# Kernel tuning notes

Measured on AMD Instinct MI355X. Metric: run time of the kernel, lower is better.

Reference implementation:

```python
import jax, jax.numpy as jnp
import numpy as np

B, N, K = 2, 2048, 30          # batch, residues, neighbors
DN, DE, L = 256, 128, 3        # dim_nodes, dim_edges, num_layers
NF, EF = 12, 28                # raw node / edge feature dims
EPS = 1e-6


def _gather(h, idx):
    # h: [B,N,D], idx: [B,N,K] -> [B,N,K,D]
    b, n, k = idx.shape
    d = h.shape[-1]
    return jnp.take_along_axis(h, idx.reshape(b, n * k, 1), axis=1).reshape(b, n, k, d)


def _nrm(v):
    return v / (jnp.linalg.norm(v, axis=-1, keepdims=True) + EPS)


def _forward(X, C, Wn, bn, We, be, Wm1, bm1, Wm2, bm2, Wue1, bue1, Wue2, bue2):
    mask_i = (C > 0).astype(X.dtype)                      # [B,N]
    Nat, CA, Cat, Oat = X[..., 0, :], X[..., 1, :], X[..., 2, :], X[..., 3, :]

    # local residue frames via Gram-Schmidt on (N, CA, C)
    u = _nrm(Cat - CA)
    v0 = Nat - CA
    v = _nrm(v0 - jnp.sum(v0 * u, -1, keepdims=True) * u)
    w = jnp.cross(u, v)
    R = jnp.stack([u, v, w], axis=-1)                     # [B,N,3,3]

    # node features: internal coords (unit bond vectors + log lengths)
    def bond_feat(bv):
        return jnp.concatenate([_nrm(bv), jnp.log(jnp.linalg.norm(bv, axis=-1, keepdims=True) + EPS)], -1)
    node_feat = jnp.concatenate([bond_feat(CA - Nat), bond_feat(Cat - CA), bond_feat(Oat - Cat)], -1)  # [B,N,12]
    node_h = (node_feat @ Wn + bn) * mask_i[..., None]

    # kNN graph on centroid distances (graph_distance_atom_type=-1)
    Xc = X.mean(axis=2)                                   # [B,N,3]
    D2 = jnp.sum((Xc[:, :, None] - Xc[:, None, :]) ** 2, -1)  # [B,N,N]
    BIG = 1e9
    D2 = D2 + BIG * (1.0 - mask_i)[:, None, :] + BIG * jnp.eye(N, dtype=X.dtype)[None]
    _, edge_idx = jax.lax.top_k(-D2, K)                   # [B,N,K]

    mask_j = _gather(mask_i[..., None], edge_idx)[..., 0]
    mask_ij = mask_i[..., None] * mask_j                  # [B,N,K]

    # edge features: RBF distances + local-frame direction + relative rotation
    xj = _gather(Xc, edge_idx)
    d = xj - Xc[:, :, None]                               # [B,N,K,3]
    dist = jnp.linalg.norm(d, axis=-1)
    local = jnp.einsum('bndc,bnkd->bnkc', R, d)           # R_i^T d
    dirv = local / (dist[..., None] + EPS)
    Rj = _gather(R.reshape(B, N, 9), edge_idx).reshape(B, N, K, 3, 3)
    Rrel = jnp.einsum('bnde,bnkdf->bnkef', R, Rj).reshape(B, N, K, 9)  # R_i^T R_j
    centers = jnp.linspace(0.0, 20.0, 16)
    sigma = 20.0 / 16.0
    rbf = jnp.exp(-(((dist[..., None] - centers) / sigma) ** 2))       # [B,N,K,16]
    edge_h = (jnp.concatenate([rbf, dirv, Rrel], -1) @ We + be) * mask_ij[..., None]

    # GNN message passing: gather -> MLP -> masked mean scatter, + edge update
    denom = jnp.sum(mask_ij, -1, keepdims=True) + EPS     # [B,N,1]
    for l in range(L):
        hj = _gather(node_h, edge_idx)                    # [B,N,K,DN]
        hi = jnp.broadcast_to(node_h[:, :, None], hj.shape)
        mi = jnp.concatenate([hi, hj, edge_h], -1)        # [B,N,K,2*DN+DE]
        m = jax.nn.softplus(mi @ Wm1[l] + bm1[l]) @ Wm2[l] + bm2[l]
        m = m * mask_ij[..., None]
        node_h = (node_h + m.sum(axis=2) / denom) * mask_i[..., None]
        e = jax.nn.softplus(mi @ Wue1[l] + bue1[l]) @ Wue2[l] + bue2[l]
        edge_h = (edge_h + e) * mask_ij[..., None]

    return node_h, edge_h, edge_idx, mask_i, mask_ij


def setup_inputs() -> dict:
    key = jax.random.key(0)
    ks = jax.random.split(key, 10)
    s = lambda i, shp: jax.random.normal(ks[i], shp, jnp.float32) * 0.05
    M = 2 * DN + DE
    inp = {
        'X': jax.random.normal(ks[0], (B, N, 4, 3), jnp.float32),
        'C': jax.random.randint(ks[1], (B, N), 0, 4),
        'Wn': s(2, (NF, DN)), 'bn': jnp.zeros((DN,), jnp.float32),
        'We': s(3, (EF, DE)), 'be': jnp.zeros((DE,), jnp.float32),
        'Wm1': s(4, (L, M, DN)), 'bm1': jnp.zeros((L, DN), jnp.float32),
        'Wm2': s(5, (L, DN, DN)), 'bm2': jnp.zeros((L, DN), jnp.float32),
        'Wue1': s(6, (L, M, DE)), 'bue1': jnp.zeros((L, DE), jnp.float32),
        'Wue2': s(7, (L, DE, DE)), 'bue2': jnp.zeros((L, DE), jnp.float32),
    }
    return inp


def reference(X, C, Wn, bn, We, be, Wm1, bm1, Wm2, bm2, Wue1, bue1, Wue2, bue2):
    return _forward(X, C, Wn, bn, We, be, Wm1, bm1, Wm2, bm2, Wue1, bue1, Wue2, bue2)
```

## Files before the change

kernel.cpp:

```cpp
#include <hip/hip_runtime.h>
#include <math.h>

#define Bdim 2
#define Nn   2048
#define Kn   30
#define KP   32
#define DNc  256
#define DEc  128
#define NODES (Bdim*Nn)
#define EDGES (Bdim*Nn*Kn)
#define RPAD  (NODES*KP)
#define EPSF 1e-6f

#define BK 64
#define LDA (BK+8)
#define LDP 136

typedef __attribute__((ext_vector_type(8))) short short8;
typedef __attribute__((ext_vector_type(4))) short sh4;
typedef __attribute__((ext_vector_type(4))) float floatx4;

__device__ __forceinline__ float softplusf(float x){
    float e = __expf(-fabsf(x));
    return fmaxf(x, 0.f) + __logf(1.f + e);
}

__device__ __forceinline__ unsigned short f2bf(float x){
    union { float f; unsigned u; } v; v.f = x;
    unsigned r = v.u + 0x7fff + ((v.u >> 16) & 1);
    return (unsigned short)(r >> 16);
}
__device__ __forceinline__ float bf2f(unsigned short h){
    union { unsigned u; float f; } v; v.u = ((unsigned)h) << 16;
    return v.f;
}

__global__ __launch_bounds__(256) void k_geom(
    const float* __restrict__ X, const int* __restrict__ C,
    float* __restrict__ Xc, float* __restrict__ Rm,
    float* __restrict__ feat, float* __restrict__ mask_out)
{
    int id = blockIdx.x*256 + threadIdx.x;
    if (id >= NODES) return;
    float a[4][3];
    #pragma unroll
    for (int t=0;t<4;++t)
        #pragma unroll
        for (int d=0;d<3;++d) a[t][d] = X[id*12 + t*3 + d];
    #pragma unroll
    for (int d=0; d<3; ++d){
        float s = __fadd_rn(__fadd_rn(__fadd_rn(a[0][d],a[1][d]),a[2][d]),a[3][d]);
        Xc[id*3+d] = __fmul_rn(s, 0.25f);
    }
    mask_out[id] = (C[id] > 0) ? 1.f : 0.f;

    float u[3], v[3], w[3], b2[3], v0[3], vv[3];
    #pragma unroll
    for (int d=0;d<3;++d) b2[d] = a[2][d]-a[1][d];
    float n2 = sqrtf(b2[0]*b2[0]+b2[1]*b2[1]+b2[2]*b2[2]);
    #pragma unroll
    for (int d=0;d<3;++d) u[d] = b2[d]/(n2+EPSF);
    #pragma unroll
    for (int d=0;d<3;++d) v0[d] = a[0][d]-a[1][d];
    float dt = v0[0]*u[0]+v0[1]*u[1]+v0[2]*u[2];
    #pragma unroll
    for (int d=0;d<3;++d) vv[d] = v0[d] - dt*u[d];
    float nv = sqrtf(vv[0]*vv[0]+vv[1]*vv[1]+vv[2]*vv[2]);
    #pragma unroll
    for (int d=0;d<3;++d) v[d] = vv[d]/(nv+EPSF);
    w[0] = u[1]*v[2]-u[2]*v[1];
    w[1] = u[2]*v[0]-u[0]*v[2];
    w[2] = u[0]*v[1]-u[1]*v[0];
    #pragma unroll
    for (int d=0;d<3;++d){
        Rm[id*9 + d*3 + 0] = u[d];
        Rm[id*9 + d*3 + 1] = v[d];
        Rm[id*9 + d*3 + 2] = w[d];
    }
    float bonds[3][3];
    #pragma unroll
    for (int d=0;d<3;++d){
        bonds[0][d] = a[1][d]-a[0][d];
        bonds[1][d] = b2[d];
        bonds[2][d] = a[3][d]-a[2][d];
    }
    #pragma unroll
    for (int bi=0;bi<3;++bi){
        float nb = sqrtf(bonds[bi][0]*bonds[bi][0]+bonds[bi][1]*bonds[bi][1]+bonds[bi][2]*bonds[bi][2]);
        #pragma unroll
        for (int d=0;d<3;++d) feat[id*12 + bi*4 + d] = bonds[bi][d]/(nb+EPSF);
        feat[id*12 + bi*4 + 3] = logf(nb+EPSF);
    }
}

__global__ __launch_bounds__(256) void k_nodeh(
    const float* __restrict__ feat, const float* __restrict__ Wn,
    const float* __restrict__ bn, const int* __restrict__ C,
    float* __restrict__ node_h, unsigned short* __restrict__ node_bf)
{
    int nid = blockIdx.x;
    int c   = threadIdx.x;
    __shared__ float f[12];
    if (c < 12) f[c] = feat[nid*12 + c];
    __syncthreads();
    float acc = bn[c];
    #pragma unroll
    for (int k=0;k<12;++k) acc += f[k]*Wn[k*DNc + c];
    float mask = (C[nid] > 0) ? 1.f : 0.f;
    float r = acc*mask;
    node_h[nid*DNc + c] = r;
    node_bf[nid*DNc + c] = f2bf(r);
}

__global__ __launch_bounds__(256) void k_knn(
    const float* __restrict__ Xc, const int* __restrict__ C,
    int* __restrict__ eidx, float* __restrict__ eidx_f)
{
    __shared__ float sx[Nn], sy[Nn], sz[Nn], sadd[Nn];
    int tid  = threadIdx.x;
    int lane = tid & 63, wave = tid >> 6;
    int node0 = blockIdx.x*4;
    int base  = (node0 >> 11) << 11;
    for (int j=tid; j<Nn; j+=256){
        int gj = base + j;
        sx[j] = Xc[gj*3+0]; sy[j] = Xc[gj*3+1]; sz[j] = Xc[gj*3+2];
        sadd[j] = (C[gj] > 0) ? 0.f : 1e9f;
    }
    __syncthreads();

    int node = node0 + wave;
    int iloc = node & (Nn-1);
    float xi = sx[iloc], yi = sy[iloc], zi = sz[iloc];

    unsigned long long kreg[32];
    unsigned long long gm[8];
    #pragma unroll
    for (int t=0; t<32; ++t){
        int j = lane + t*64;
        float dx = __fsub_rn(xi, sx[j]);
        float dy = __fsub_rn(yi, sy[j]);
        float dz = __fsub_rn(zi, sz[j]);
        float vv = __fadd_rn(__fadd_rn(__fmul_rn(dx,dx),__fmul_rn(dy,dy)),__fmul_rn(dz,dz));
        vv = __fadd_rn(vv, sadd[j]);
        if (j == iloc) vv = __fadd_rn(vv, 1e9f);
        union { float f; unsigned u; } cv; cv.f = vv;
        kreg[t] = (((unsigned long long)cv.u) << 11) | (unsigned)j;
    }
    #pragma unroll
    for (int g=0; g<8; ++g){
        unsigned long long a = kreg[4*g+0], b = kreg[4*g+1];
        unsigned long long c = kreg[4*g+2], d = kreg[4*g+3];
        unsigned long long m1 = a<b?a:b, m2 = c<d?c:d;
        gm[g] = m1<m2?m1:m2;
    }
    unsigned long long m = gm[0]; int marg = 0;
    #pragma unroll
    for (int g=1; g<8; ++g) if (gm[g] < m){ m = gm[g]; marg = g; }

    for (int kk=0; kk<Kn; ++kk){
        unsigned long long best = m;
        #pragma unroll
        for (int d=1; d<64; d<<=1){
            unsigned long long o = __shfl_xor(best, d, 64);
            if (o < best) best = o;
        }
        if (lane == 0){
            int j = (int)(best & 2047ull);
            eidx  [(size_t)node*Kn + kk] = j;
            eidx_f[(size_t)node*Kn + kk] = (float)j;
        }
        if (m == best){
            #pragma unroll
            for (int g=0; g<8; ++g){
                if (marg == g){
                    #pragma unroll
                    for (int t=0; t<4; ++t)
                        if (kreg[4*g+t] == best) kreg[4*g+t] = ~0ull;
                    unsigned long long a = kreg[4*g+0], b = kreg[4*g+1];
                    unsigned long long c = kreg[4*g+2], d = kreg[4*g+3];
                    unsigned long long m1 = a<b?a:b, m2 = c<d?c:d;
                    gm[g] = m1<m2?m1:m2;
                }
            }
            m = gm[0]; marg = 0;
            #pragma unroll
            for (int g=1; g<8; ++g) if (gm[g] < m){ m = gm[g]; marg = g; }
        }
    }
}

__global__ __launch_bounds__(256) void k_edge(
    const float* __restrict__ Xc, const float* __restrict__ Rm,
    const int* __restrict__ eidx, const int* __restrict__ C,
    const float* __restrict__ We, const float* __restrict__ be,
    unsigned short* __restrict__ edge_pad, float* __restrict__ mask_ij_out,
    float* __restrict__ mask_pad, int* __restrict__ jg_pad,
    float* __restrict__ cnt)
{
    __shared__ float sWe[28*128];
    __shared__ float sbe[128];
    __shared__ float sfeat[30][28];
    __shared__ float smij[30];
    __shared__ float sRi[9];
    int nid = blockIdx.x;
    int b   = nid >> 11;
    int tid = threadIdx.x;
    for (int idx=tid; idx<28*128; idx+=256) sWe[idx] = We[idx];
    if (tid < 128) sbe[tid] = be[tid];
    if (tid < 9)   sRi[tid] = Rm[nid*9 + tid];
    __syncthreads();
    if (tid < KP){
        if (tid < Kn){
            int e  = nid*Kn + tid;
            int j  = eidx[e];
            int jb = (b<<11) + j;
            jg_pad[nid*KP + tid] = jb;
            float d0 = Xc[jb*3+0]-Xc[nid*3+0];
            float d1 = Xc[jb*3+1]-Xc[nid*3+1];
            float d2v= Xc[jb*3+2]-Xc[nid*3+2];
            float dist = sqrtf(d0*d0+d1*d1+d2v*d2v);
            float mij = (C[nid] > 0 && C[jb] > 0) ? 1.f : 0.f;
            smij[tid] = mij;
            mask_ij_out[e] = mij;
            mask_pad[nid*KP + tid] = mij;
            #pragma unroll
            for (int c=0; c<16; ++c){
                float ctr = (20.f/15.f)*(float)c;
                float t = (dist - ctr)*(1.f/1.25f);
                sfeat[tid][c] = expf(-t*t);
            }
            #pragma unroll
            for (int cc=0; cc<3; ++cc){
                float loc = sRi[0*3+cc]*d0 + sRi[1*3+cc]*d1 + sRi[2*3+cc]*d2v;
                sfeat[tid][16+cc] = loc/(dist+EPSF);
            }
            float rj[9];
            #pragma unroll
            for (int q=0;q<9;++q) rj[q] = Rm[jb*9+q];
            #pragma unroll
            for (int ee=0; ee<3; ++ee)
                #pragma unroll
                for (int ff=0; ff<3; ++ff)
                    sfeat[tid][19+ee*3+ff] = sRi[0+ee]*rj[0+ff] + sRi[3+ee]*rj[3+ff] + sRi[6+ee]*rj[6+ff];
        } else {
            jg_pad[nid*KP + tid] = nid;
            mask_pad[nid*KP + tid] = 0.f;
        }
    }
    __syncthreads();
    if (tid == 0){
        float c = 0.f;
        #pragma unroll
        for (int k=0;k<Kn;++k) c += smij[k];
        cnt[nid] = c;
    }
    int c  = tid & 127;
    int eg = tid >> 7;
    for (int k=eg; k<KP; k+=2){
        if (k < Kn){
            float acc = sbe[c];
            #pragma unroll
            for (int f=0; f<28; ++f) acc += sfeat[k][f]*sWe[f*128 + c];
            edge_pad[(size_t)(nid*KP + k)*DEc + c] = f2bf(acc * smij[k]);
        } else {
            edge_pad[(size_t)(nid*KP + k)*DEc + c] = 0;
        }
    }
}

__global__ __launch_bounds__(256) void k_pack_pqw(
    const float* __restrict__ Wm1, const float* __restrict__ Wue1,
    unsigned short* __restrict__ wPQw)
{
    int id = blockIdx.x*256 + threadIdx.x;
    if (id >= 3*768*256) return;
    int l = id / (768*256);
    int rem = id % (768*256);
    int n = rem >> 8, k = rem & 255;
    int c = (n < 384) ? n : n - 384;
    int r = (n < 384) ? k : 256 + k;
    float v = (c < 256) ? Wm1[((size_t)l*640 + r)*256 + c]
                        : Wue1[((size_t)l*640 + r)*128 + (c-256)];
    wPQw[id] = f2bf(v);
}

__global__ __launch_bounds__(256) void k_pack_ew(
    const float* __restrict__ Wm1, const float* __restrict__ Wue1,
    unsigned short* __restrict__ wEw)
{
    int id = blockIdx.x*256 + threadIdx.x;
    if (id >= 3*384*128) return;
    int l = id / (384*128);
    int rem = id % (384*128);
    int n = rem >> 7, k = rem & 127;
    int r = 512 + k;
    float v = (n < 256) ? Wm1[((size_t)l*640 + r)*256 + n]
                        : Wue1[((size_t)l*640 + r)*128 + (n-256)];
    wEw[id] = f2bf(v);
}

__global__ __launch_bounds__(256) void k_pack_ue2(
    const float* __restrict__ Wue2, unsigned short* __restrict__ wUe2w)
{
    int id = blockIdx.x*256 + threadIdx.x;
    if (id >= 3*128*128) return;
    int l = id / (128*128);
    int rem = id % (128*128);
    int n = rem >> 7, k = rem & 127;
    wUe2w[id] = f2bf(Wue2[((size_t)l*128 + k)*128 + n]);
}

__global__ __launch_bounds__(256) void k_pack_m2(
    const float* __restrict__ Wm2, unsigned short* __restrict__ wM2w)
{
    int id = blockIdx.x*256 + threadIdx.x;
    if (id >= 3*256*256) return;
    int l = id / (256*256);
    int rem = id % (256*256);
    int n = rem >> 8, k = rem & 255;
    wM2w[id] = f2bf(Wm2[((size_t)l*256 + k)*256 + n]);
}

__device__ __forceinline__ void stage_tile(
    const unsigned short* __restrict__ gbase, int ldg, int k0,
    unsigned short* lds, int tid)
{
    #pragma unroll
    for (int it=0; it<4; ++it){
        int idx = it*256 + tid;
        int row = idx >> 3;
        int ke  = (idx & 7) * 8;
        const float4* src = (const float4*)(gbase + (size_t)row*ldg + k0 + ke);
        *(float4*)(&lds[row*LDA + ke]) = *src;
    }
}

__device__ __forceinline__ void mma_tile(
    const unsigned short* Als, const unsigned short* Bls,
    int wm, int wn, int lane, floatx4 acc[4][4])
{
    #pragma unroll
    for (int s=0; s<2; ++s){
        short8 af[4], bf[4];
        int kidx = s*32 + (lane>>4)*8;
        #pragma unroll
        for (int t=0;t<4;++t){
            int row = wm*64 + t*16 + (lane&15);
            af[t] = *(const short8*)(&Als[row*LDA + kidx]);
            int col = wn*64 + t*16 + (lane&15);
            bf[t] = *(const short8*)(&Bls[col*LDA + kidx]);
        }
        #pragma unroll
        for (int i=0;i<4;++i)
            #pragma unroll
            for (int j=0;j<4;++j)
                acc[i][j] = __builtin_amdgcn_mfma_f32_16x16x32_bf16(af[i], bf[j], acc[i][j], 0,0,0);
    }
}

__device__ __forceinline__ void mma_tileA_lp(
    const unsigned short* Atile, const unsigned short* Bls,
    int k0, int wm, int wn, int lane, floatx4 acc[4][4])
{
    #pragma unroll
    for (int s=0; s<2; ++s){
        short8 af[4], bf[4];
        int kloc = s*32 + (lane>>4)*8;
        #pragma unroll
        for (int t=0;t<4;++t){
            int row = wm*64 + t*16 + (lane&15);
            af[t] = *(const short8*)(&Atile[row*LDP + k0 + kloc]);
            int col = wn*64 + t*16 + (lane&15);
            bf[t] = *(const short8*)(&Bls[col*LDA + kloc]);
        }
        #pragma unroll
        for (int i=0;i<4;++i)
            #pragma unroll
            for (int j=0;j<4;++j)
                acc[i][j] = __builtin_amdgcn_mfma_f32_16x16x32_bf16(af[i], bf[j], acc[i][j], 0,0,0);
    }
}

__global__ __launch_bounds__(256) void k_pq(
    const unsigned short* __restrict__ A, const unsigned short* __restrict__ Bw,
    unsigned short* __restrict__ PQbf,
    const float* __restrict__ bm1l, const float* __restrict__ bue1l)
{
    __shared__ __align__(16) unsigned short smem[2*128*LDA];
    unsigned short* Als = smem;
    unsigned short* Bls = smem + 128*LDA;
    unsigned short* tile = smem;
    int tid = threadIdx.x;
    int lane = tid & 63, wave = tid >> 6;
    int wm = wave >> 1, wn = wave & 1;
    const unsigned short* Ab = A + (size_t)blockIdx.x*128*256;
    const unsigned short* Bb = Bw + (size_t)blockIdx.y*128*256;
    floatx4 acc[4][4];
    #pragma unroll
    for (int i=0;i<4;++i)
        #pragma unroll
        for (int j=0;j<4;++j) acc[i][j] = (floatx4){0.f,0.f,0.f,0.f};
    for (int k0=0; k0<256; k0+=BK){
        stage_tile(Ab, 256, k0, Als, tid);
        stage_tile(Bb, 256, k0, Bls, tid);
        __syncthreads();
        mma_tile(Als, Bls, wm, wn, lane, acc);
        __syncthreads();
    }
    int quad = lane >> 4, cl = lane & 15;
    #pragma unroll
    for (int i=0;i<4;++i){
        #pragma unroll
        for (int rg=0;rg<4;++rg){
            int rowl = wm*64 + i*16 + quad*4 + rg;
            #pragma unroll
            for (int j=0;j<4;++j){
                int coll = wn*64 + j*16 + cl;
                int col  = blockIdx.y*128 + coll;
                float biasv = 0.f;
                if (col < 256)       biasv = bm1l[col];
                else if (col < 384)  biasv = bue1l[col-256];
                tile[rowl*LDP + coll] = f2bf(acc[i][j][rg] + biasv);
            }
        }
    }
    __syncthreads();
    {
        int rl = tid >> 1;
        int h  = tid & 1;
        unsigned short* dst = PQbf + (size_t)(blockIdx.x*128 + rl)*768 + blockIdx.y*128 + h*64;
        #pragma unroll
        for (int q=0; q<8; ++q)
            *(short8*)(dst + q*8) = *(const short8*)(&tile[rl*LDP + h*64 + q*8]);
    }
}

__global__ __launch_bounds__(256) void k_h1s(
    const unsigned short* __restrict__ Apad, const unsigned short* __restrict__ Bw,
    const unsigned short* __restrict__ PQbf, const int* __restrict__ jg_pad,
    const float* __restrict__ mask_pad,
    unsigned short* __restrict__ Sout)
{
    __shared__ __align__(16) unsigned short smem[2*128*LDA];
    __shared__ float smask[128];
    unsigned short* Als = smem;
    unsigned short* Bls = smem + 128*LDA;
    unsigned short* pqT = smem;

    int tid = threadIdx.x;
    int lane = tid & 63, wave = tid >> 6;
    int wm = wave >> 1, wn = wave & 1;
    int colblk = blockIdx.y;

    const unsigned short* Ab = Apad + (size_t)blockIdx.x*128*128;
    const unsigned short* Bb = Bw + (size_t)colblk*128*128;
    floatx4 acc[4][4];
    #pragma unroll
    for (int i=0;i<4;++i)
        #pragma unroll
        for (int j=0;j<4;++j) acc[i][j] = (floatx4){0.f,0.f,0.f,0.f};
    for (int k0=0; k0<128; k0+=BK){
        stage_tile(Ab, 128, k0, Als, tid);
        stage_tile(Bb, 128, k0, Bls, tid);
        __syncthreads();
        mma_tile(Als, Bls, wm, wn, lane, acc);
        __syncthreads();
    }

    {
        int colbase = colblk*128;
        #pragma unroll
        for (int it=0; it<2; ++it){
            int w    = it*256 + tid;
            int rq   = w & 31;
            int c8   = w >> 5;
            int row0 = rq*4;
            int r0   = blockIdx.x*128 + row0;
            int ni   = r0 >> 5;
            int4 jg4 = *(const int4*)&jg_pad[r0];
            int colg = colbase + c8*8;
            short8 pv = *(const short8*)(PQbf + (size_t)ni*768 + colg);
            short8 q0 = *(const short8*)(PQbf + (size_t)jg4.x*768 + 384 + colg);
            short8 q1 = *(const short8*)(PQbf + (size_t)jg4.y*768 + 384 + colg);
            short8 q2 = *(const short8*)(PQbf + (size_t)jg4.z*768 + 384 + colg);
            short8 q3 = *(const short8*)(PQbf + (size_t)jg4.w*768 + 384 + colg);
            #pragma unroll
            for (int q=0; q<8; ++q){
                float pf = bf2f((unsigned short)pv[q]);
                sh4 ov;
                ov[0] = (short)f2bf(pf + bf2f((unsigned short)q0[q]));
                ov[1] = (short)f2bf(pf + bf2f((unsigned short)q1[q]));
                ov[2] = (short)f2bf(pf + bf2f((unsigned short)q2[q]));
                ov[3] = (short)f2bf(pf + bf2f((unsigned short)q3[q]));
                *(sh4*)(&pqT[(c8*8 + q)*LDP + row0]) = ov;
            }
        }
        if (tid < 128) smask[tid] = mask_pad[blockIdx.x*128 + tid];
    }
    __syncthreads();

    int quad = lane >> 4, cl = lane & 15;
    float sumA[4] = {0.f,0.f,0.f,0.f};
    float sumB[4] = {0.f,0.f,0.f,0.f};
    #pragma unroll
    for (int i=0;i<4;++i){
        int rowl0 = wm*64 + i*16 + quad*4;
        float4 mk = *(const float4*)&smask[rowl0];
        float mkv[4] = {mk.x, mk.y, mk.z, mk.w};
        #pragma unroll
        for (int j=0;j<4;++j){
            int coll = wn*64 + j*16 + cl;
            sh4 pq4 = *(const sh4*)(&pqT[coll*LDP + rowl0]);
            #pragma unroll
            for (int rg=0; rg<4; ++rg){
                float v  = softplusf(acc[i][j][rg] + bf2f((unsigned short)pq4[rg]));
                float mv = mkv[rg]*v;
                if (i < 2) sumA[j] += mv; else sumB[j] += mv;
            }
        }
    }

    int nodeA = blockIdx.x*4 + wm*2;
    #pragma unroll
    for (int j=0;j<4;++j){
        float a = sumA[j];
        a += __shfl_xor(a, 16, 64);
        a += __shfl_xor(a, 32, 64);
        float b = sumB[j];
        b += __shfl_xor(b, 16, 64);
        b += __shfl_xor(b, 32, 64);
        int col = colblk*128 + wn*64 + j*16 + cl;
        if (quad == 0)      Sout[(size_t)nodeA*256 + col]     = f2bf(a);
        else if (quad == 1) Sout[(size_t)(nodeA+1)*256 + col] = f2bf(b);
    }
}

__global__ __launch_bounds__(256) void k_h1e(
    const unsigned short* __restrict__ Apad, const unsigned short* __restrict__ BwE,
    const unsigned short* __restrict__ BwU2,
    const unsigned short* __restrict__ PQbf, const int* __restrict__ jg_pad,
    const float* __restrict__ mask_pad, const float* __restrict__ bue2l,
    unsigned short* __restrict__ edge_pad, float* __restrict__ edge_f32,
    int writeF32)
{
    __shared__ __align__(16) unsigned short smem[3*128*LDA];
    __shared__ float sbias[128];
    unsigned short* Als  = smem;
    unsigned short* Bls  = smem + 128*LDA;
    unsigned short* B2   = smem + 2*128*LDA;
    unsigned short* tile = smem;

    int tid = threadIdx.x;
    int lane = tid & 63, wave = tid >> 6;
    int wm = wave >> 1, wn = wave & 1;
    if (tid < 128) sbias[tid] = bue2l[tid];

    const unsigned short* Ab = Apad + (size_t)blockIdx.x*128*128;
    floatx4 acc[4][4];
    #pragma unroll
    for (int i=0;i<4;++i)
        #pragma unroll
        for (int j=0;j<4;++j) acc[i][j] = (floatx4){0.f,0.f,0.f,0.f};
    for (int k0=0; k0<128; k0+=BK){
        stage_tile(Ab, 128, k0, Als, tid);
        stage_tile(BwE, 128, k0, Bls, tid);
        __syncthreads();
        mma_tile(Als, Bls, wm, wn, lane, acc);
        __syncthreads();
    }

    {
        int rl = tid >> 1;
        int h  = tid & 1;
        int r  = blockIdx.x*128 + rl;
        int ni = r >> 5;
        int jg = jg_pad[r];
        int cb = 256 + h*64;
        const unsigned short* Pr = PQbf + (size_t)ni*768 + cb;
        const unsigned short* Qr = PQbf + (size_t)jg*768 + 384 + cb;
        #pragma unroll
        for (int q=0; q<8; ++q){
            short8 pv = *(const short8*)(Pr + q*8);
            short8 qv = *(const short8*)(Qr + q*8);
            short8 ov;
            #pragma unroll
            for (int z=0; z<8; ++z)
                ov[z] = (short)f2bf(bf2f((unsigned short)pv[z]) + bf2f((unsigned short)qv[z]));
            *(short8*)(&tile[rl*LDP + h*64 + q*8]) = ov;
        }
    }
    __syncthreads();

    int quad = lane >> 4, cl = lane & 15;
    #pragma unroll
    for (int i=0;i<4;++i){
        #pragma unroll
        for (int rg=0;rg<4;++rg){
            int rowl = wm*64 + i*16 + quad*4 + rg;
            #pragma unroll
            for (int j=0;j<4;++j){
                int coll = wn*64 + j*16 + cl;
                float pq = bf2f(tile[rowl*LDP + coll]);
                float v  = softplusf(acc[i][j][rg] + pq);
                tile[rowl*LDP + coll] = f2bf(v);
            }
        }
    }
    __syncthreads();

    floatx4 acc2[4][4];
    #pragma unroll
    for (int i=0;i<4;++i)
        #pragma unroll
        for (int j=0;j<4;++j) acc2[i][j] = (floatx4){0.f,0.f,0.f,0.f};
    for (int k0=0; k0<128; k0+=BK){
        stage_tile(BwU2, 128, k0, B2, tid);
        __syncthreads();
        mma_tileA_lp(tile, B2, k0, wm, wn, lane, acc2);
        __syncthreads();
    }

    #pragma unroll
    for (int i=0;i<4;++i){
        #pragma unroll
        for (int rg=0;rg<4;++rg){
            int rowl = wm*64 + i*16 + quad*4 + rg;
            #pragma unroll
            for (int j=0;j<4;++j){
                int coll = wn*64 + j*16 + cl;
                tile[rowl*LDP + coll] = f2bf(acc2[i][j][rg]);
            }
        }
    }
    __syncthreads();

    {
        int rl = tid >> 1;
        int h  = tid & 1;
        int r  = blockIdx.x*128 + rl;
        int k  = r & (KP-1);
        if (k < Kn){
            float mij = mask_pad[r];
            int node = r >> 5;
            int e = node*Kn + k;
            unsigned short* ep = edge_pad + (size_t)r*128 + h*64;
            float* fp = edge_f32 + (size_t)e*128 + h*64;
            #pragma unroll
            for (int q=0; q<8; ++q){
                short8 ov = *(const short8*)(ep + q*8);
                short8 av = *(const short8*)(&tile[rl*LDP + h*64 + q*8]);
                float4 b0 = *(const float4*)(&sbias[h*64 + q*8]);
                float4 b1 = *(const float4*)(&sbias[h*64 + q*8 + 4]);
                float nv[8];
                nv[0] = (bf2f((unsigned short)ov[0]) + bf2f((unsigned short)av[0]) + b0.x)*mij;
                nv[1] = (bf2f((unsigned short)ov[1]) + bf2f((unsigned short)av[1]) + b0.y)*mij;
                nv[2] = (bf2f((unsigned short)ov[2]) + bf2f((unsigned short)av[2]) + b0.z)*mij;
                nv[3] = (bf2f((unsigned short)ov[3]) + bf2f((unsigned short)av[3]) + b0.w)*mij;
                nv[4] = (bf2f((unsigned short)ov[4]) + bf2f((unsigned short)av[4]) + b1.x)*mij;
                nv[5] = (bf2f((unsigned short)ov[5]) + bf2f((unsigned short)av[5]) + b1.y)*mij;
                nv[6] = (bf2f((unsigned short)ov[6]) + bf2f((unsigned short)av[6]) + b1.z)*mij;
                nv[7] = (bf2f((unsigned short)ov[7]) + bf2f((unsigned short)av[7]) + b1.w)*mij;
                short8 sv;
                #pragma unroll
                for (int z=0; z<8; ++z) sv[z] = (short)f2bf(nv[z]);
                *(short8*)(ep + q*8) = sv;
                if (writeF32){
                    float4 f0 = {nv[0],nv[1],nv[2],nv[3]};
                    float4 f1 = {nv[4],nv[5],nv[6],nv[7]};
                    *(float4*)(fp + q*8)     = f0;
                    *(float4*)(fp + q*8 + 4) = f1;
                }
            }
        }
    }
}

__global__ __launch_bounds__(256) void k_node_gemm(
    const unsigned short* __restrict__ S, const unsigned short* __restrict__ Bw,
    const float* __restrict__ bm2l, const float* __restrict__ cnt,
    const float* __restrict__ mask_i,
    float* __restrict__ node_h, unsigned short* __restrict__ node_bf)
{
    __shared__ __align__(16) unsigned short Als[128*LDA];
    __shared__ __align__(16) unsigned short Bls[128*LDA];
    int tid = threadIdx.x;
    int lane = tid & 63, wave = tid >> 6;
    int wm = wave >> 1, wn = wave & 1;
    const unsigned short* Ab = S + (size_t)blockIdx.x*128*256;
    const unsigned short* Bb = Bw + (size_t)blockIdx.y*128*256;
    floatx4 acc[4][4];
    #pragma unroll
    for (int i=0;i<4;++i)
        #pragma unroll
        for (int j=0;j<4;++j) acc[i][j] = (floatx4){0.f,0.f,0.f,0.f};
    for (int k0=0; k0<256; k0+=BK){
        stage_tile(Ab, 256, k0, Als, tid);
        stage_tile(Bb, 256, k0, Bls, tid);
        __syncthreads();
        mma_tile(Als, Bls, wm, wn, lane, acc);
        __syncthreads();
    }
    int quad = lane >> 4, cl = lane & 15;
    #pragma unroll
    for (int i=0;i<4;++i){
        #pragma unroll
        for (int rg=0;rg<4;++rg){
            int nid = blockIdx.x*128 + wm*64 + i*16 + quad*4 + rg;
            float ct = cnt[nid];
            float mi = mask_i[nid];
            #pragma unroll
            for (int j=0;j<4;++j){
                int col = blockIdx.y*128 + wn*64 + j*16 + cl;
                float msum = acc[i][j][rg] + ct*bm2l[col];
                float nh = node_h[(size_t)nid*256 + col];
                float r = (nh + msum/(ct+EPSF))*mi;
                node_h[(size_t)nid*256 + col] = r;
                node_bf[(size_t)nid*256 + col] = f2bf(r);
            }
        }
    }
}

extern "C" void kernel_launch(void* const* d_in, const int* in_sizes, int n_in,
                              void* d_out, int out_size, void* d_ws, size_t ws_size,
                              hipStream_t stream)
{
    (void)in_sizes; (void)n_in; (void)out_size; (void)ws_size;
    const float* X   = (const float*)d_in[0];
    const int*   C   = (const int*)  d_in[1];
    const float* Wn  = (const float*)d_in[2];
    const float* bn  = (const float*)d_in[3];
    const float* We  = (const float*)d_in[4];
    const float* be  = (const float*)d_in[5];
    const float* Wm1 = (const float*)d_in[6];
    const float* bm1 = (const float*)d_in[7];
    const float* Wm2 = (const float*)d_in[8];
    const float* bm2 = (const float*)d_in[9];
    const float* Wue1= (const float*)d_in[10];
    const float* bue1= (const float*)d_in[11];
    const float* Wue2= (const float*)d_in[12];
    const float* bue2= (const float*)d_in[13];

    float* out       = (float*)d_out;
    float* out_node  = out;
    float* out_edge  = out + 1048576;
    float* out_eidxf = out + 16777216;
    float* out_maski = out + 16900096;
    float* out_maskij= out + 16904192;

    char* wsb = (char*)d_ws;
    size_t off = 0;
    float* wXc    = (float*)(wsb + off); off += (size_t)12288*4;
    float* wR     = (float*)(wsb + off); off += (size_t)36864*4;
    float* wF     = (float*)(wsb + off); off += (size_t)49152*4;
    int*   wEidx  = (int*)  (wsb + off); off += (size_t)EDGES*4;
    int*   wJgPad = (int*)  (wsb + off); off += (size_t)RPAD*4;
    float* wMaskP = (float*)(wsb + off); off += (size_t)RPAD*4;
    float* wCnt   = (float*)(wsb + off); off += (size_t)NODES*4;
    unsigned short* wPQ      = (unsigned short*)(wsb + off); off += (size_t)NODES*768*2;
    unsigned short* wS       = (unsigned short*)(wsb + off); off += (size_t)NODES*256*2;
    unsigned short* wNodeBf  = (unsigned short*)(wsb + off); off += (size_t)NODES*256*2;
    unsigned short* wEdgePad = (unsigned short*)(wsb + off); off += (size_t)RPAD*128*2;
    unsigned short* wPQw     = (unsigned short*)(wsb + off); off += (size_t)3*768*256*2;
    unsigned short* wEw      = (unsigned short*)(wsb + off); off += (size_t)3*384*128*2;
    unsigned short* wUe2w    = (unsigned short*)(wsb + off); off += (size_t)3*128*128*2;
    unsigned short* wM2w     = (unsigned short*)(wsb + off); off += (size_t)3*256*256*2;

    k_geom <<<16,    256, 0, stream>>>(X, C, wXc, wR, wF, out_maski);
    k_nodeh<<<NODES, 256, 0, stream>>>(wF, Wn, bn, C, out_node, wNodeBf);
    k_knn  <<<NODES/4, 256, 0, stream>>>(wXc, C, wEidx, out_eidxf);
    k_edge <<<NODES, 256, 0, stream>>>(wXc, wR, wEidx, C, We, be,
                                       wEdgePad, out_maskij, wMaskP, wJgPad, wCnt);

    k_pack_pqw<<<(3*768*256+255)/256, 256, 0, stream>>>(Wm1, Wue1, wPQw);
    k_pack_ew <<<(3*384*128+255)/256, 256, 0, stream>>>(Wm1, Wue1, wEw);
    k_pack_ue2<<<(3*128*128+255)/256, 256, 0, stream>>>(Wue2, wUe2w);
    k_pack_m2 <<<(3*256*256+255)/256, 256, 0, stream>>>(Wm2, wM2w);

    for (int l=0; l<3; ++l){
        k_pq<<<dim3(32,6), 256, 0, stream>>>(wNodeBf, wPQw + (size_t)l*768*256, wPQ,
                                             bm1 + l*256, bue1 + l*128);
        k_h1s<<<dim3(RPAD/128,2), 256, 0, stream>>>(
            wEdgePad, wEw + (size_t)l*384*128, wPQ, wJgPad, wMaskP, wS);
        k_h1e<<<RPAD/128, 256, 0, stream>>>(
            wEdgePad, wEw + (size_t)l*384*128 + (size_t)256*128,
            wUe2w + (size_t)l*128*128, wPQ, wJgPad, wMaskP, bue2 + l*128,
            wEdgePad, out_edge, (l==2) ? 1 : 0);
        k_node_gemm<<<dim3(NODES/128,2), 256, 0, stream>>>(
            wS, wM2w + (size_t)l*256*256, bm2 + l*256, wCnt, out_maski,
            out_node, wNodeBf);
    }
}
```

Before: 545.0 us.

## Shrink node GEMM tiles, cut k_h1e LDS, and split last-layer edge epilogue

```diff
diff --git a/kernel.cpp b/kernel.cpp
--- a/kernel.cpp
+++ b/kernel.cpp
@@ -321,12 +321,13 @@
     wM2w[id] = f2bf(Wm2[((size_t)l*256 + k)*256 + n]);
 }
 
-__device__ __forceinline__ void stage_tile(
+template<int NR>
+__device__ __forceinline__ void stage_tile_t(
     const unsigned short* __restrict__ gbase, int ldg, int k0,
     unsigned short* lds, int tid)
 {
     #pragma unroll
-    for (int it=0; it<4; ++it){
+    for (int it=0; it<NR/32; ++it){
         int idx = it*256 + tid;
         int row = idx >> 3;
         int ke  = (idx & 7) * 8;
@@ -335,25 +336,29 @@
     }
 }
 
-__device__ __forceinline__ void mma_tile(
+template<int TI, int TJ>
+__device__ __forceinline__ void mma_tile_t(
     const unsigned short* Als, const unsigned short* Bls,
-    int wm, int wn, int lane, floatx4 acc[4][4])
+    int wm, int wn, int lane, floatx4 acc[TI][TJ])
 {
     #pragma unroll
     for (int s=0; s<2; ++s){
-        short8 af[4], bf[4];
+        short8 af[TI], bf[TJ];
         int kidx = s*32 + (lane>>4)*8;
         #pragma unroll
-        for (int t=0;t<4;++t){
-            int row = wm*64 + t*16 + (lane&15);
+        for (int t=0;t<TI;++t){
+            int row = wm*(TI*16) + t*16 + (lane&15);
             af[t] = *(const short8*)(&Als[row*LDA + kidx]);
-            int col = wn*64 + t*16 + (lane&15);
+        }
+        #pragma unroll
+        for (int t=0;t<TJ;++t){
+            int col = wn*(TJ*16) + t*16 + (lane&15);
             bf[t] = *(const short8*)(&Bls[col*LDA + kidx]);
         }
         #pragma unroll
-        for (int i=0;i<4;++i)
-            #pragma unroll
-            for (int j=0;j<4;++j)
+        for (int i=0;i<TI;++i)
+            #pragma unroll
+            for (int j=0;j<TJ;++j)
                 acc[i][j] = __builtin_amdgcn_mfma_f32_16x16x32_bf16(af[i], bf[j], acc[i][j], 0,0,0);
     }
 }
@@ -386,33 +391,33 @@
     unsigned short* __restrict__ PQbf,
     const float* __restrict__ bm1l, const float* __restrict__ bue1l)
 {
-    __shared__ __align__(16) unsigned short smem[2*128*LDA];
+    __shared__ __align__(16) unsigned short smem[(64+128)*LDA];
     unsigned short* Als = smem;
-    unsigned short* Bls = smem + 128*LDA;
+    unsigned short* Bls = smem + 64*LDA;
     unsigned short* tile = smem;
     int tid = threadIdx.x;
     int lane = tid & 63, wave = tid >> 6;
     int wm = wave >> 1, wn = wave & 1;
-    const unsigned short* Ab = A + (size_t)blockIdx.x*128*256;
+    const unsigned short* Ab = A + (size_t)blockIdx.x*64*256;
     const unsigned short* Bb = Bw + (size_t)blockIdx.y*128*256;
-    floatx4 acc[4][4];
-    #pragma unroll
-    for (int i=0;i<4;++i)
+    floatx4 acc[2][4];
+    #pragma unroll
+    for (int i=0;i<2;++i)
         #pragma unroll
         for (int j=0;j<4;++j) acc[i][j] = (floatx4){0.f,0.f,0.f,0.f};
     for (int k0=0; k0<256; k0+=BK){
-        stage_tile(Ab, 256, k0, Als, tid);
-        stage_tile(Bb, 256, k0, Bls, tid);
+        stage_tile_t<64>(Ab, 256, k0, Als, tid);
+        stage_tile_t<128>(Bb, 256, k0, Bls, tid);
         __syncthreads();
-        mma_tile(Als, Bls, wm, wn, lane, acc);
+        mma_tile_t<2,4>(Als, Bls, wm, wn, lane, acc);
         __syncthreads();
     }
     int quad = lane >> 4, cl = lane & 15;
     #pragma unroll
-    for (int i=0;i<4;++i){
+    for (int i=0;i<2;++i){
         #pragma unroll
         for (int rg=0;rg<4;++rg){
-            int rowl = wm*64 + i*16 + quad*4 + rg;
+            int rowl = wm*32 + i*16 + quad*4 + rg;
             #pragma unroll
             for (int j=0;j<4;++j){
                 int coll = wn*64 + j*16 + cl;
@@ -426,12 +431,12 @@
     }
     __syncthreads();
     {
-        int rl = tid >> 1;
-        int h  = tid & 1;
-        unsigned short* dst = PQbf + (size_t)(blockIdx.x*128 + rl)*768 + blockIdx.y*128 + h*64;
-        #pragma unroll
-        for (int q=0; q<8; ++q)
-            *(short8*)(dst + q*8) = *(const short8*)(&tile[rl*LDP + h*64 + q*8]);
+        int rl = tid >> 2;
+        int h  = tid & 3;
+        unsigned short* dst = PQbf + (size_t)(blockIdx.x*64 + rl)*768 + blockIdx.y*128 + h*32;
+        #pragma unroll
+        for (int q=0; q<4; ++q)
+            *(short8*)(dst + q*8) = *(const short8*)(&tile[rl*LDP + h*32 + q*8]);
     }
 }
 
@@ -460,10 +465,10 @@
         #pragma unroll
         for (int j=0;j<4;++j) acc[i][j] = (floatx4){0.f,0.f,0.f,0.f};
     for (int k0=0; k0<128; k0+=BK){
-        stage_tile(Ab, 128, k0, Als, tid);
-        stage_tile(Bb, 128, k0, Bls, tid);
+        stage_tile_t<128>(Ab, 128, k0, Als, tid);
+        stage_tile_t<128>(Bb, 128, k0, Bls, tid);
         __syncthreads();
-        mma_tile(Als, Bls, wm, wn, lane, acc);
+        mma_tile_t<4,4>(Als, Bls, wm, wn, lane, acc);
         __syncthreads();
     }
 
@@ -541,19 +546,17 @@
     const unsigned short* __restrict__ PQbf, const int* __restrict__ jg_pad,
     const float* __restrict__ mask_pad, const float* __restrict__ bue2l,
     unsigned short* __restrict__ edge_pad, float* __restrict__ edge_f32,
-    int writeF32)
-{
-    __shared__ __align__(16) unsigned short smem[3*128*LDA];
-    __shared__ float sbias[128];
+    int last)
+{
+    __shared__ __align__(16) unsigned short smem[26624];
     unsigned short* Als  = smem;
     unsigned short* Bls  = smem + 128*LDA;
-    unsigned short* B2   = smem + 2*128*LDA;
     unsigned short* tile = smem;
+    unsigned short* B2   = smem + 128*LDP;
 
     int tid = threadIdx.x;
     int lane = tid & 63, wave = tid >> 6;
     int wm = wave >> 1, wn = wave & 1;
-    if (tid < 128) sbias[tid] = bue2l[tid];
 
     const unsigned short* Ab = Apad + (size_t)blockIdx.x*128*128;
     floatx4 acc[4][4];
@@ -562,12 +565,14 @@
         #pragma unroll
         for (int j=0;j<4;++j) acc[i][j] = (floatx4){0.f,0.f,0.f,0.f};
     for (int k0=0; k0<128; k0+=BK){
-        stage_tile(Ab, 128, k0, Als, tid);
-        stage_tile(BwE, 128, k0, Bls, tid);
+        stage_tile_t<128>(Ab, 128, k0, Als, tid);
+        stage_tile_t<128>(BwE, 128, k0, Bls, tid);
         __syncthreads();
-        mma_tile(Als, Bls, wm, wn, lane, acc);
+        mma_tile_t<4,4>(Als, Bls, wm, wn, lane, acc);
         __syncthreads();
     }
+
+    stage_tile_t<128>(BwU2, 128, 0, B2, tid);
 
     {
         int rl = tid >> 1;
@@ -613,13 +618,14 @@
     for (int i=0;i<4;++i)
         #pragma unroll
         for (int j=0;j<4;++j) acc2[i][j] = (floatx4){0.f,0.f,0.f,0.f};
-    for (int k0=0; k0<128; k0+=BK){
-        stage_tile(BwU2, 128, k0, B2, tid);
-        __syncthreads();
-        mma_tileA_lp(tile, B2, k0, wm, wn, lane, acc2);
-        __syncthreads();
-    }
-
+    mma_tileA_lp(tile, B2, 0, wm, wn, lane, acc2);
+    __syncthreads();
+    stage_tile_t<128>(BwU2, 128, 64, B2, tid);
+    __syncthreads();
+    mma_tileA_lp(tile, B2, 64, wm, wn, lane, acc2);
+    __syncthreads();
+
+    float* sbias = (float*)B2;
     #pragma unroll
     for (int i=0;i<4;++i){
         #pragma unroll
@@ -632,25 +638,47 @@
             }
         }
     }
-    __syncthreads();
-
-    {
-        int rl = tid >> 1;
-        int h  = tid & 1;
-        int r  = blockIdx.x*128 + rl;
-        int k  = r & (KP-1);
-        if (k < Kn){
-            float mij = mask_pad[r];
-            int node = r >> 5;
-            int e = node*Kn + k;
-            unsigned short* ep = edge_pad + (size_t)r*128 + h*64;
-            float* fp = edge_f32 + (size_t)e*128 + h*64;
-            #pragma unroll
-            for (int q=0; q<8; ++q){
-                short8 ov = *(const short8*)(ep + q*8);
-                short8 av = *(const short8*)(&tile[rl*LDP + h*64 + q*8]);
-                float4 b0 = *(const float4*)(&sbias[h*64 + q*8]);
-                float4 b1 = *(const float4*)(&sbias[h*64 + q*8 + 4]);
+    if (tid < 128) sbias[tid] = bue2l[tid];
+    __syncthreads();
+
+    if (last){
+        int c16  = lane & 31;
+        int rsub = lane >> 5;
+        #pragma unroll
+        for (int step=0; step<16; ++step){
+            int rowl = wave*32 + step*2 + rsub;
+            int R = blockIdx.x*128 + rowl;
+            int k = R & (KP-1);
+            if (k < Kn){
+                float mij = mask_pad[R];
+                int node = R >> 5;
+                int e = node*Kn + k;
+                sh4 ov = *(const sh4*)(edge_pad + (size_t)R*128 + c16*4);
+                sh4 av = *(const sh4*)(&tile[rowl*LDP + c16*4]);
+                float4 bv = *(const float4*)(&sbias[c16*4]);
+                float4 f;
+                f.x = (bf2f((unsigned short)ov[0]) + bf2f((unsigned short)av[0]) + bv.x)*mij;
+                f.y = (bf2f((unsigned short)ov[1]) + bf2f((unsigned short)av[1]) + bv.y)*mij;
+                f.z = (bf2f((unsigned short)ov[2]) + bf2f((unsigned short)av[2]) + bv.z)*mij;
+                f.w = (bf2f((unsigned short)ov[3]) + bf2f((unsigned short)av[3]) + bv.w)*mij;
+                *(float4*)(edge_f32 + (size_t)e*128 + c16*4) = f;
+            }
+        }
+    } else {
+        int c8   = lane & 15;
+        int rsub = lane >> 4;
+        #pragma unroll
+        for (int step=0; step<8; ++step){
+            int rowl = wave*32 + step*4 + rsub;
+            int R = blockIdx.x*128 + rowl;
+            int k = R & (KP-1);
+            if (k < Kn){
+                float mij = mask_pad[R];
+                unsigned short* ep = edge_pad + (size_t)R*128 + c8*8;
+                short8 ov = *(const short8*)ep;
+                short8 av = *(const short8*)(&tile[rowl*LDP + c8*8]);
+                float4 b0 = *(const float4*)(&sbias[c8*8]);
+                float4 b1 = *(const float4*)(&sbias[c8*8 + 4]);
                 float nv[8];
                 nv[0] = (bf2f((unsigned short)ov[0]) + bf2f((unsigned short)av[0]) + b0.x)*mij;
                 nv[1] = (bf2f((unsigned short)ov[1]) + bf2f((unsigned short)av[1]) + b0.y)*mij;
@@ -663,13 +691,7 @@
                 short8 sv;
                 #pragma unroll
                 for (int z=0; z<8; ++z) sv[z] = (short)f2bf(nv[z]);
-                *(short8*)(ep + q*8) = sv;
-                if (writeF32){
-                    float4 f0 = {nv[0],nv[1],nv[2],nv[3]};
-                    float4 f1 = {nv[4],nv[5],nv[6],nv[7]};
-                    *(float4*)(fp + q*8)     = f0;
-                    *(float4*)(fp + q*8 + 4) = f1;
-                }
+                *(short8*)ep = sv;
             }
         }
     }
@@ -681,36 +703,36 @@
     const float* __restrict__ mask_i,
     float* __restrict__ node_h, unsigned short* __restrict__ node_bf)
 {
-    __shared__ __align__(16) unsigned short Als[128*LDA];
-    __shared__ __align__(16) unsigned short Bls[128*LDA];
+    __shared__ __align__(16) unsigned short Als[64*LDA];
+    __shared__ __align__(16) unsigned short Bls[64*LDA];
     int tid = threadIdx.x;
     int lane = tid & 63, wave = tid >> 6;
     int wm = wave >> 1, wn = wave & 1;
-    const unsigned short* Ab = S + (size_t)blockIdx.x*128*256;
-    const unsigned short* Bb = Bw + (size_t)blockIdx.y*128*256;
-    floatx4 acc[4][4];
-    #pragma unroll
-    for (int i=0;i<4;++i)
-        #pragma unroll
-        for (int j=0;j<4;++j) acc[i][j] = (floatx4){0.f,0.f,0.f,0.f};
+    const unsigned short* Ab = S + (size_t)blockIdx.x*64*256;
+    const unsigned short* Bb = Bw + (size_t)blockIdx.y*64*256;
+    floatx4 acc[2][2];
+    #pragma unroll
+    for (int i=0;i<2;++i)
+        #pragma unroll
+        for (int j=0;j<2;++j) acc[i][j] = (floatx4){0.f,0.f,0.f,0.f};
     for (int k0=0; k0<256; k0+=BK){
-        stage_tile(Ab, 256, k0, Als, tid);
-        stage_tile(Bb, 256, k0, Bls, tid);
+        stage_tile_t<64>(Ab, 256, k0, Als, tid);
+        stage_tile_t<64>(Bb, 256, k0, Bls, tid);
         __syncthreads();
-        mma_tile(Als, Bls, wm, wn, lane, acc);
+        mma_tile_t<2,2>(Als, Bls, wm, wn, lane, acc);
         __syncthreads();
     }
     int quad = lane >> 4, cl = lane & 15;
     #pragma unroll
-    for (int i=0;i<4;++i){
+    for (int i=0;i<2;++i){
         #pragma unroll
         for (int rg=0;rg<4;++rg){
-            int nid = blockIdx.x*128 + wm*64 + i*16 + quad*4 + rg;
+            int nid = blockIdx.x*64 + wm*32 + i*16 + quad*4 + rg;
             float ct = cnt[nid];
             float mi = mask_i[nid];
             #pragma unroll
-            for (int j=0;j<4;++j){
-                int col = blockIdx.y*128 + wn*64 + j*16 + cl;
+            for (int j=0;j<2;++j){
+                int col = blockIdx.y*64 + wn*32 + j*16 + cl;
                 float msum = acc[i][j][rg] + ct*bm2l[col];
                 float nh = node_h[(size_t)nid*256 + col];
                 float r = (nh + msum/(ct+EPSF))*mi;
@@ -778,7 +800,7 @@
     k_pack_m2 <<<(3*256*256+255)/256, 256, 0, stream>>>(Wm2, wM2w);
 
     for (int l=0; l<3; ++l){
-        k_pq<<<dim3(32,6), 256, 0, stream>>>(wNodeBf, wPQw + (size_t)l*768*256, wPQ,
+        k_pq<<<dim3(64,6), 256, 0, stream>>>(wNodeBf, wPQw + (size_t)l*768*256, wPQ,
                                              bm1 + l*256, bue1 + l*128);
         k_h1s<<<dim3(RPAD/128,2), 256, 0, stream>>>(
             wEdgePad, wEw + (size_t)l*384*128, wPQ, wJgPad, wMaskP, wS);
@@ -786,7 +808,7 @@
             wEdgePad, wEw + (size_t)l*384*128 + (size_t)256*128,
             wUe2w + (size_t)l*128*128, wPQ, wJgPad, wMaskP, bue2 + l*128,
             wEdgePad, out_edge, (l==2) ? 1 : 0);
-        k_node_gemm<<<dim3(NODES/128,2), 256, 0, stream>>>(
+        k_node_gemm<<<dim3(NODES/64,4), 256, 0, stream>>>(
             wS, wM2w + (size_t)l*256*256, bm2 + l*256, wCnt, out_maski,
             out_node, wNodeBf);
     }
```

Measured after the change: 509.7 us. -6.5%, faster.
